# Performance work log

Hardware: AMD Instinct MI355X
Metric: run time of the kernel (lower is better)

## Reference

```python
import jax, jax.numpy as jnp
import numpy as np

B, Hh, Ww, C = 32, 56, 56, 256
WIN, SHIFT, HEADS = 7, 3, 8
N = WIN * WIN
nW = (Hh // WIN) * (Ww // WIN)


def _rel_pos_index(w):
    coords = np.stack(np.meshgrid(np.arange(w), np.arange(w), indexing='ij'))  # (2,w,w)
    flat = coords.reshape(2, -1)
    rel = (flat[:, :, None] - flat[:, None, :]).transpose(1, 2, 0)  # (N,N,2)
    rel[..., 0] += w - 1
    rel[..., 1] += w - 1
    rel[..., 0] *= 2 * w - 1
    return rel.sum(-1)  # (N,N) int


def _shift_attn_mask(H, W, w, s):
    img = np.zeros((H, W))
    cnt = 0
    for hs in (slice(0, -w), slice(-w, -s), slice(-s, None)):
        for ws in (slice(0, -w), slice(-w, -s), slice(-s, None)):
            img[hs, ws] = cnt
            cnt += 1
    mw = img.reshape(H // w, w, W // w, w).transpose(0, 2, 1, 3).reshape(-1, w * w)  # (nW,N)
    diff = mw[:, None, :] - mw[:, :, None]
    return np.where(diff != 0, -100.0, 0.0).astype(np.float32)  # (nW,N,N)


REL_IDX = jnp.asarray(_rel_pos_index(WIN))


def layer_norm(x, g, b):
    m = x.mean(-1, keepdims=True)
    v = ((x - m) ** 2).mean(-1, keepdims=True)
    return (x - m) / jnp.sqrt(v + 1e-5) * g + b


def setup_inputs() -> dict:
    key = jax.random.key(0)
    ks = jax.random.split(key, 10)
    s02 = 0.02
    x = jax.random.normal(ks[0], (B, Hh * Ww, C), jnp.float32)
    qkv_w = jax.random.normal(ks[1], (3 * C, C), jnp.float32) * s02
    qkv_b = jnp.zeros((3 * C,), jnp.float32)
    rpb_table = jax.random.normal(ks[2], ((2 * WIN - 1) ** 2, HEADS), jnp.float32) * s02
    proj_w = jax.random.normal(ks[3], (C, C), jnp.float32) * s02
    proj_b = jnp.zeros((C,), jnp.float32)
    fc1_w = jax.random.normal(ks[4], (4 * C, C), jnp.float32) * s02
    fc1_b = jnp.zeros((4 * C,), jnp.float32)
    fc2_w = jax.random.normal(ks[5], (C, 4 * C), jnp.float32) * s02
    fc2_b = jnp.zeros((C,), jnp.float32)
    attn_mask = jnp.asarray(_shift_attn_mask(Hh, Ww, WIN, SHIFT))
    # saliency masks: per-token binary fg/bg -> additive 0/-100 key masks
    fg_tok = jax.random.bernoulli(ks[6], 0.5, (B * nW, N))
    sal_fg = jnp.where(fg_tok[:, None, :], 0.0, -100.0) * jnp.ones((1, N, 1), jnp.float32)
    sal_bg = jnp.where(fg_tok[:, None, :], -100.0, 0.0) * jnp.ones((1, N, 1), jnp.float32)
    return dict(x=x, qkv_w=qkv_w, qkv_b=qkv_b, rpb_table=rpb_table, proj_w=proj_w,
                proj_b=proj_b, norm1_g=jnp.ones((C,)), norm1_b=jnp.zeros((C,)),
                norm2_g=jnp.ones((C,)), norm2_b=jnp.zeros((C,)),
                fc1_w=fc1_w, fc1_b=fc1_b, fc2_w=fc2_w, fc2_b=fc2_b,
                attn_mask=attn_mask, sal_fg_attn_mask=sal_fg.astype(jnp.float32),
                sal_bg_attn_mask=sal_bg.astype(jnp.float32))


def reference(x, qkv_w, qkv_b, rpb_table, proj_w, proj_b, norm1_g, norm1_b,
              norm2_g, norm2_b, fc1_w, fc1_b, fc2_w, fc2_b,
              attn_mask, sal_fg_attn_mask, sal_bg_attn_mask):
    Bb, L, Cc = x.shape
    d = Cc // HEADS
    scale = d ** -0.5
    shortcut = x
    xn = layer_norm(x, norm1_g, norm1_b).reshape(Bb, Hh, Ww, Cc)
    xs = jnp.roll(xn, (-SHIFT, -SHIFT), axis=(1, 2))
    # window partition -> (B*nW, N, C)
    nh = Hh // WIN
    xw = xs.reshape(Bb, nh, WIN, nh, WIN, Cc).transpose(0, 1, 3, 2, 4, 5).reshape(-1, N, Cc)
    B_ = xw.shape[0]
    qkv = (xw @ qkv_w.T + qkv_b).reshape(B_, N, 3, HEADS, d).transpose(2, 0, 3, 1, 4)
    q, k, v = qkv[0] * scale, qkv[1], qkv[2]  # (B_, h, N, d)
    attn = jnp.einsum('bhnd,bhmd->bhnm', q, k)
    rpb = rpb_table[REL_IDX.reshape(-1)].reshape(N, N, HEADS).transpose(2, 0, 1)
    attn = attn + rpb[None]
    attn_fg = attn + sal_fg_attn_mask[:, None]
    attn_bg = attn + sal_bg_attn_mask[:, None]

    def add_shift(a):
        a = a.reshape(B_ // nW, nW, HEADS, N, N) + attn_mask[None, :, None]
        return a.reshape(B_, HEADS, N, N)

    p = jax.nn.softmax(add_shift(attn), axis=-1)
    p_fg = jax.nn.softmax(add_shift(attn_fg), axis=-1)
    p_bg = jax.nn.softmax(add_shift(attn_bg), axis=-1)
    o = jnp.einsum('bhnm,bhmd->bhnd', p + p_fg - p_bg, v)
    o = o.transpose(0, 2, 1, 3).reshape(B_, N, Cc)
    o = o @ proj_w.T + proj_b
    # window reverse + reverse shift
    xr = o.reshape(Bb, nh, nh, WIN, WIN, Cc).transpose(0, 1, 3, 2, 4, 5).reshape(Bb, Hh, Ww, Cc)
    xr = jnp.roll(xr, (SHIFT, SHIFT), axis=(1, 2)).reshape(Bb, L, Cc)
    x = shortcut + xr
    h = layer_norm(x, norm2_g, norm2_b)
    h = jax.nn.gelu(h @ fc1_w.T + fc1_b, approximate=False) @ fc2_w.T + fc2_b
    return x + h
```

## Files before the change

kernel.cpp:

```cpp
#include <hip/hip_runtime.h>
#include <hip/hip_bf16.h>

#define HH 56
#define WWD 56
#define WIN 7
#define SHIFT 3
#define HEADS 8
#define NTOK 49
#define NW 64
#define CDIM 256
#define DH 32
#define MROWS 100352
#define SCALE_Q 0.17677669529663687f

typedef float floatx4 __attribute__((ext_vector_type(4)));
typedef __bf16 bf16x8 __attribute__((ext_vector_type(8)));

__device__ __forceinline__ float wave_sum(float v) {
#pragma unroll
    for (int m = 1; m < 64; m <<= 1) v += __shfl_xor(v, m);
    return v;
}

__device__ __forceinline__ void glds16(const void* g, void* l) {
    __builtin_amdgcn_global_load_lds(
        (const __attribute__((address_space(1))) void*)g,
        (__attribute__((address_space(3))) void*)l, 16, 0, 0);
}

__global__ __launch_bounds__(256) void convert_weights_kernel(
    const float* __restrict__ qkv_w, const float* __restrict__ proj_w,
    const float* __restrict__ fc1_w, const float* __restrict__ fc2_w,
    __hip_bfloat16* __restrict__ dst)
{
    int i = blockIdx.x * 256 + threadIdx.x;
    float v;
    if (i < 196608)       v = qkv_w[i];
    else if (i < 262144)  v = proj_w[i - 196608];
    else if (i < 524288)  v = fc1_w[i - 262144];
    else                  v = fc2_w[i - 524288];
    dst[i] = __float2bfloat16(v);
}

template <bool SHIFTED>
__global__ __launch_bounds__(256) void ln_kernel(
    const float* __restrict__ x, const float* __restrict__ g,
    const float* __restrict__ bb, __hip_bfloat16* __restrict__ out)
{
    const int tok  = blockIdx.x * 4 + (threadIdx.x >> 6);
    const int lane = threadIdx.x & 63;
    const int c    = lane * 4;

    float4 v = *reinterpret_cast<const float4*>(x + (size_t)tok * CDIM + c);
    float s = v.x + v.y + v.z + v.w;
    s = wave_sum(s);
    const float mean = s * (1.0f / 256.0f);
    float d0 = v.x - mean, d1 = v.y - mean, d2 = v.z - mean, d3 = v.w - mean;
    float sq = d0 * d0 + d1 * d1 + d2 * d2 + d3 * d3;
    sq = wave_sum(sq);
    const float rstd = rsqrtf(sq * (1.0f / 256.0f) + 1e-5f);

    float4 gv = *reinterpret_cast<const float4*>(g + c);
    float4 bv = *reinterpret_cast<const float4*>(bb + c);

    union { __hip_bfloat16 h[4]; uint2 u; } pk;
    pk.h[0] = __float2bfloat16(d0 * rstd * gv.x + bv.x);
    pk.h[1] = __float2bfloat16(d1 * rstd * gv.y + bv.y);
    pk.h[2] = __float2bfloat16(d2 * rstd * gv.z + bv.z);
    pk.h[3] = __float2bfloat16(d3 * rstd * gv.w + bv.w);

    size_t oidx;
    if (SHIFTED) {
        int b = tok / 3136;
        int l = tok - b * 3136;
        int h = l / WWD, w = l - (l / WWD) * WWD;
        int hp = h - SHIFT; if (hp < 0) hp += HH;
        int wp = w - SHIFT; if (wp < 0) wp += WWD;
        int bwin = b * NW + (hp / WIN) * 8 + (wp / WIN);
        int n = (hp % WIN) * WIN + (wp % WIN);
        oidx = ((size_t)bwin * NTOK + n) * CDIM + c;
    } else {
        oidx = (size_t)tok * CDIM + c;
    }
    *reinterpret_cast<uint2*>(out + oidx) = pk.u;
}

template <int MODE>
__global__ __launch_bounds__(256) void gemm_kernel(
    const __hip_bfloat16* __restrict__ A,
    const __hip_bfloat16* __restrict__ Wt,
    const float* __restrict__ bias,
    void* __restrict__ outv,
    const float* __restrict__ aux,
    int M, int Nn, int K)
{
    __shared__ __hip_bfloat16 As[3][128 * 32];
    __shared__ __hip_bfloat16 Bs[3][128 * 32];

    const int t = threadIdx.x;
    const int wave = t >> 6, lane = t & 63;

    const int nwg  = gridDim.x * gridDim.y;
    const int orig = blockIdx.y * gridDim.x + blockIdx.x;
    const int q = nwg >> 3, r = nwg & 7;
    const int xcd = orig & 7, loc = orig >> 3;
    const int lin = (xcd < r ? xcd * (q + 1) : r * (q + 1) + (xcd - r) * q) + loc;
    const int bx = lin % gridDim.x;
    const int by = lin / gridDim.x;

    const int m0 = by * 128, n0 = bx * 128;
    const int wr = (wave >> 1) * 64;
    const int wc = (wave & 1) * 64;

    floatx4 acc[4][4] = {};

    const int c0 = wave * 64 + lane;
    const int c1 = 256 + c0;
    const int r0 = c0 >> 2, p0 = c0 & 3, g0 = p0 ^ ((r0 >> 1) & 3);
    const int r1 = c1 >> 2, p1 = c1 & 3, g1 = p1 ^ ((r1 >> 1) & 3);
    const __hip_bfloat16* gA0 = A  + (size_t)(m0 + r0) * K + g0 * 8;
    const __hip_bfloat16* gA1 = A  + (size_t)(m0 + r1) * K + g1 * 8;
    const __hip_bfloat16* gB0 = Wt + (size_t)(n0 + r0) * K + g0 * 8;
    const __hip_bfloat16* gB1 = Wt + (size_t)(n0 + r1) * K + g1 * 8;
    const int base0 = (wave * 64) * 8;
    const int base1 = (256 + wave * 64) * 8;

    const int fm = lane & 15;
    const int g4 = lane >> 4;

    const int nt = K >> 5;

    glds16(gA0,      As[0] + base0);
    glds16(gA1,      As[0] + base1);
    glds16(gB0,      Bs[0] + base0);
    glds16(gB1,      Bs[0] + base1);
    glds16(gA0 + 32, As[1] + base0);
    glds16(gA1 + 32, As[1] + base1);
    glds16(gB0 + 32, Bs[1] + base0);
    glds16(gB1 + 32, Bs[1] + base1);
    asm volatile("s_waitcnt vmcnt(4)" ::: "memory");
    __builtin_amdgcn_s_barrier();
    __builtin_amdgcn_sched_barrier(0);

    int cur = 0;
    for (int tt = 0; tt < nt; ++tt) {
        if (tt + 2 < nt) {
            const int nx2 = (cur >= 1) ? cur - 1 : cur + 2;
            const int k2 = (tt + 2) << 5;
            glds16(gA0 + k2, As[nx2] + base0);
            glds16(gA1 + k2, As[nx2] + base1);
            glds16(gB0 + k2, Bs[nx2] + base0);
            glds16(gB1 + k2, Bs[nx2] + base1);
        }

        const __hip_bfloat16* Ac = As[cur];
        const __hip_bfloat16* Bc = Bs[cur];
        bf16x8 af[4], bfr[4];
#pragma unroll
        for (int mt = 0; mt < 4; ++mt) {
            const int ml = wr + mt * 16 + fm;
            af[mt] = *reinterpret_cast<const bf16x8*>(
                Ac + ml * 32 + ((g4 ^ ((ml >> 1) & 3)) * 8));
            const int nl = wc + mt * 16 + fm;
            bfr[mt] = *reinterpret_cast<const bf16x8*>(
                Bc + nl * 32 + ((g4 ^ ((nl >> 1) & 3)) * 8));
        }
#pragma unroll
        for (int mt = 0; mt < 4; ++mt)
#pragma unroll
            for (int nn = 0; nn < 4; ++nn)
                acc[mt][nn] = __builtin_amdgcn_mfma_f32_16x16x32_bf16(
                    af[mt], bfr[nn], acc[mt][nn], 0, 0, 0);

        if (tt + 1 < nt) {
            if (tt + 2 < nt)
                asm volatile("s_waitcnt vmcnt(4) lgkmcnt(0)" ::: "memory");
            else
                asm volatile("s_waitcnt vmcnt(0) lgkmcnt(0)" ::: "memory");
            __builtin_amdgcn_s_barrier();
            __builtin_amdgcn_sched_barrier(0);
        }
        cur = (cur >= 2) ? 0 : cur + 1;
    }

    float bv[4];
#pragma unroll
    for (int nn = 0; nn < 4; ++nn) bv[nn] = bias[n0 + wc + nn * 16 + fm];

#pragma unroll
    for (int mt = 0; mt < 4; ++mt) {
#pragma unroll
        for (int rr = 0; rr < 4; ++rr) {
            const int m_g = m0 + wr + mt * 16 + g4 * 4 + rr;
            size_t row_idx = 0;
            if (MODE == 1) {
                int bwin = m_g / NTOK;
                int ntok = m_g - bwin * NTOK;
                int b = bwin >> 6, wi = bwin & 63;
                int r2 = ntok / WIN, cc = ntok - r2 * WIN;
                int hp = (wi >> 3) * WIN + r2;
                int wp = (wi & 7) * WIN + cc;
                int h = hp + SHIFT; if (h >= HH) h -= HH;
                int w = wp + SHIFT; if (w >= WWD) w -= WWD;
                row_idx = ((size_t)b * 3136 + h * WWD + w) * CDIM;
            }
#pragma unroll
            for (int nn = 0; nn < 4; ++nn) {
                const int n_g = n0 + wc + nn * 16 + fm;
                float val = acc[mt][nn][rr] + bv[nn];
                if (MODE == 0) {
                    if (n_g < 256) val *= SCALE_Q;
                    reinterpret_cast<__hip_bfloat16*>(outv)[(size_t)m_g * Nn + n_g] =
                        __float2bfloat16(val);
                } else if (MODE == 2) {
                    float u  = val;
                    float y2 = 1.5957691216057308f * u
                             * (1.0f + 0.044715f * u * u);
                    float e  = __expf(y2);
                    float th = 1.0f - 2.0f / (e + 1.0f);
                    float gl = 0.5f * u * (1.0f + th);
                    reinterpret_cast<__hip_bfloat16*>(outv)[(size_t)m_g * Nn + n_g] =
                        __float2bfloat16(gl);
                } else if (MODE == 3) {
                    size_t idx = (size_t)m_g * CDIM + n_g;
                    reinterpret_cast<float*>(outv)[idx] = aux[idx] + val;
                } else {
                    size_t idx = row_idx + n_g;
                    reinterpret_cast<float*>(outv)[idx] = aux[idx] + val;
                }
            }
        }
    }
}

__global__ __launch_bounds__(256) void attn_kernel(
    const __hip_bfloat16* __restrict__ qkv,
    const float* __restrict__ rpb_table,
    const float* __restrict__ sal_fg,
    __hip_bfloat16* __restrict__ o)
{
    __shared__ unsigned short Pl[4][64 * 40];
    __shared__ unsigned short Vt[4][32 * 72];
    __shared__ float rpb_l[4][176];

    const int t = threadIdx.x;
    const int wave = t >> 6, lane = t & 63;
    const int lane15 = lane & 15, g4 = lane >> 4;
    const int b_ = blockIdx.x >> 1;
    const int h = ((blockIdx.x & 1) << 2) | wave;

    unsigned short* Pw = Pl[wave];
    unsigned short* Vw = Vt[wave];
    float* rpbw = rpb_l[wave];

    const unsigned short* qkv_u = reinterpret_cast<const unsigned short*>(qkv);
    const size_t base = (size_t)b_ * (NTOK * 768) + h * DH;

#pragma unroll
    for (int it = 0; it < 32; ++it) {
        int idx = it * 64 + lane;
        int key = idx >> 5, d = idx & 31;
        unsigned short v = (key < NTOK) ? qkv_u[base + key * 768 + 512 + d]
                                        : (unsigned short)0;
        Vw[d * 72 + key] = v;
    }
#pragma unroll
    for (int it = 0; it < 3; ++it) {
        int i = it * 64 + lane;
        if (i < 169) rpbw[i] = rpb_table[i * 8 + h];
    }
    float sfv = (lane < NTOK) ? sal_fg[(size_t)b_ * (NTOK * NTOK) + lane] : -100.f;
    const unsigned long long fgmask = __ballot(sfv == 0.0f);

    bf16x8 kf[4], qf[4];
#pragma unroll
    for (int mt = 0; mt < 4; ++mt)
        kf[mt] = *reinterpret_cast<const bf16x8*>(
            qkv_u + base + (size_t)(mt * 16 + lane15) * 768 + 256 + g4 * 8);
#pragma unroll
    for (int nt = 0; nt < 4; ++nt)
        qf[nt] = *reinterpret_cast<const bf16x8*>(
            qkv_u + base + (size_t)(nt * 16 + lane15) * 768 + g4 * 8);

    floatx4 S[4][4] = {};
#pragma unroll
    for (int mt = 0; mt < 4; ++mt)
#pragma unroll
        for (int nt = 0; nt < 4; ++nt)
            S[mt][nt] = __builtin_amdgcn_mfma_f32_16x16x32_bf16(
                kf[mt], qf[nt], S[mt][nt], 0, 0, 0);

    const int wr_ = (b_ & 63) >> 3, wc_ = (b_ & 63) & 7;
    int qlin[4], qreg[4];
#pragma unroll
    for (int nt = 0; nt < 4; ++nt) {
        int q = nt * 16 + lane15;
        int qr = (q * 147) >> 10, qc = q - qr * 7;
        qlin[nt] = q + 6 * qr + 84;
        qreg[nt] = ((wr_ == 7) ? ((qr < 4) ? 1 : 2) : 0) * 3
                 + ((wc_ == 7) ? ((qc < 4) ? 1 : 2) : 0);
    }

#pragma unroll
    for (int mt = 0; mt < 4; ++mt)
#pragma unroll
        for (int r = 0; r < 4; ++r) {
            int key = mt * 16 + g4 * 4 + r;
            int kr = (key * 147) >> 10, kc = key - kr * 7;
            int klin = key + 6 * kr;
            int kreg = ((wr_ == 7) ? ((kr < 4) ? 1 : 2) : 0) * 3
                     + ((wc_ == 7) ? ((kc < 4) ? 1 : 2) : 0);
            bool pad = key >= NTOK;
#pragma unroll
            for (int nt = 0; nt < 4; ++nt) {
                int idx = qlin[nt] - klin;
                idx = idx < 0 ? 0 : (idx > 168 ? 168 : idx);
                float s = S[mt][nt][r] + rpbw[idx]
                        + ((qreg[nt] == kreg) ? 0.f : -100.f);
                S[mt][nt][r] = pad ? -1e30f : s;
            }
        }

    float Cfg[4], Cbg[4];
#pragma unroll
    for (int nt = 0; nt < 4; ++nt) {
        float mfg = -3e38f, mbg = -3e38f;
#pragma unroll
        for (int mt = 0; mt < 4; ++mt)
#pragma unroll
            for (int r = 0; r < 4; ++r) {
                int key = mt * 16 + g4 * 4 + r;
                bool fg = (fgmask >> key) & 1ULL;
                float s = S[mt][nt][r];
                mfg = fg ? fmaxf(mfg, s) : mfg;
                mbg = fg ? mbg : fmaxf(mbg, s);
            }
        mfg = fmaxf(mfg, __shfl_xor(mfg, 16)); mfg = fmaxf(mfg, __shfl_xor(mfg, 32));
        mbg = fmaxf(mbg, __shfl_xor(mbg, 16)); mbg = fmaxf(mbg, __shfl_xor(mbg, 32));
        float t1 = 0.f, t2 = 0.f;
#pragma unroll
        for (int mt = 0; mt < 4; ++mt)
#pragma unroll
            for (int r = 0; r < 4; ++r) {
                int key = mt * 16 + g4 * 4 + r;
                bool fg = (fgmask >> key) & 1ULL;
                float e = __expf(S[mt][nt][r] - (fg ? mfg : mbg));
                S[mt][nt][r] = e;
                t1 += fg ? e : 0.f;
                t2 += fg ? 0.f : e;
            }
        t1 += __shfl_xor(t1, 16); t1 += __shfl_xor(t1, 32);
        t2 += __shfl_xor(t2, 16); t2 += __shfl_xor(t2, 32);
        const float m0 = fmaxf(mfg, mbg);
        const float m1 = fmaxf(mfg, mbg - 100.f);
        const float m2 = fmaxf(mfg - 100.f, mbg);
        const float a1 = __expf(mfg - m0),          a2 = __expf(mbg - m0);
        const float b1 = __expf(mfg - m1),          b2 = __expf(mbg - 100.f - m1);
        const float c1 = __expf(mfg - 100.f - m2),  c2 = __expf(mbg - m2);
        const float r0 = 1.f / (t1 * a1 + t2 * a2);
        const float r1 = 1.f / (t1 * b1 + t2 * b2);
        const float r2 = 1.f / (t1 * c1 + t2 * c2);
        Cfg[nt] = a1 * r0 + b1 * r1 - c1 * r2;
        Cbg[nt] = a2 * r0 + b2 * r1 - c2 * r2;
    }

    floatx4 Oc[4][2] = {};
#pragma unroll
    for (int kc = 0; kc < 2; ++kc) {
#pragma unroll
        for (int mh = 0; mh < 2; ++mh) {
            const int mt = kc * 2 + mh;
#pragma unroll
            for (int rp = 0; rp < 2; ++rp) {
                const int key0 = mt * 16 + g4 * 4 + 2 * rp;
                const bool fg0 = (fgmask >> key0) & 1ULL;
                const bool fg1 = (fgmask >> (key0 + 1)) & 1ULL;
                const int keyLocal = key0 - kc * 32;
#pragma unroll
                for (int nt = 0; nt < 4; ++nt) {
                    float pA = S[mt][nt][2 * rp]     * (fg0 ? Cfg[nt] : Cbg[nt]);
                    float pB = S[mt][nt][2 * rp + 1] * (fg1 ? Cfg[nt] : Cbg[nt]);
                    union { __hip_bfloat16 hh[2]; unsigned u; } pk;
                    pk.hh[0] = __float2bfloat16(pA);
                    pk.hh[1] = __float2bfloat16(pB);
                    const int q = nt * 16 + lane15;
                    *reinterpret_cast<unsigned*>(Pw + q * 40 + keyLocal) = pk.u;
                }
            }
        }
        bf16x8 pa[4], vb[2];
#pragma unroll
        for (int mtile = 0; mtile < 4; ++mtile)
            pa[mtile] = *reinterpret_cast<const bf16x8*>(
                Pw + (mtile * 16 + lane15) * 40 + g4 * 8);
#pragma unroll
        for (int n2 = 0; n2 < 2; ++n2)
            vb[n2] = *reinterpret_cast<const bf16x8*>(
                Vw + (n2 * 16 + lane15) * 72 + kc * 32 + g4 * 8);
#pragma unroll
        for (int mtile = 0; mtile < 4; ++mtile)
#pragma unroll
            for (int n2 = 0; n2 < 2; ++n2)
                Oc[mtile][n2] = __builtin_amdgcn_mfma_f32_16x16x32_bf16(
                    pa[mtile], vb[n2], Oc[mtile][n2], 0, 0, 0);
    }

#pragma unroll
    for (int mt = 0; mt < 4; ++mt)
#pragma unroll
        for (int r = 0; r < 4; ++r) {
            int query = mt * 16 + g4 * 4 + r;
            if (query < NTOK) {
                __hip_bfloat16* op = o + ((size_t)b_ * NTOK + query) * CDIM + h * DH;
#pragma unroll
                for (int n2 = 0; n2 < 2; ++n2)
                    op[n2 * 16 + lane15] = __float2bfloat16(Oc[mt][n2][r]);
            }
        }
}

extern "C" void kernel_launch(void* const* d_in, const int* in_sizes, int n_in,
                              void* d_out, int out_size, void* d_ws, size_t ws_size,
                              hipStream_t stream)
{
    const float* x        = (const float*)d_in[0];
    const float* qkv_w    = (const float*)d_in[1];
    const float* qkv_b    = (const float*)d_in[2];
    const float* rpb_tab  = (const float*)d_in[3];
    const float* proj_w   = (const float*)d_in[4];
    const float* proj_b   = (const float*)d_in[5];
    const float* n1g      = (const float*)d_in[6];
    const float* n1b      = (const float*)d_in[7];
    const float* n2g      = (const float*)d_in[8];
    const float* n2b      = (const float*)d_in[9];
    const float* fc1_w    = (const float*)d_in[10];
    const float* fc1_b    = (const float*)d_in[11];
    const float* fc2_w    = (const float*)d_in[12];
    const float* fc2_b    = (const float*)d_in[13];
    const float* sal_fg   = (const float*)d_in[15];

    char* ws = (char*)d_ws;
    __hip_bfloat16* regA = (__hip_bfloat16*)ws;
    __hip_bfloat16* regB = (__hip_bfloat16*)(ws + 205520896);
    float*          x2   = (float*)(ws + 205520896 + 51380224);
    __hip_bfloat16* wbf  = (__hip_bfloat16*)(ws + 205520896 + 51380224 + 102760448);
    __hip_bfloat16* wqkv  = wbf;
    __hip_bfloat16* wproj = wbf + 196608;
    __hip_bfloat16* wfc1  = wbf + 262144;
    __hip_bfloat16* wfc2  = wbf + 524288;

    convert_weights_kernel<<<3072, 256, 0, stream>>>(qkv_w, proj_w, fc1_w, fc2_w, wbf);

    ln_kernel<true><<<MROWS / 4, 256, 0, stream>>>(x, n1g, n1b, regB);

    gemm_kernel<0><<<dim3(768 / 128, MROWS / 128), 256, 0, stream>>>(
        regB, wqkv, qkv_b, regA, nullptr, MROWS, 768, 256);

    attn_kernel<<<2048 * 2, 256, 0, stream>>>(regA, rpb_tab, sal_fg, regB);

    gemm_kernel<1><<<dim3(256 / 128, MROWS / 128), 256, 0, stream>>>(
        regB, wproj, proj_b, x2, x, MROWS, 256, 256);

    ln_kernel<false><<<MROWS / 4, 256, 0, stream>>>(x2, n2g, n2b, regB);

    gemm_kernel<2><<<dim3(1024 / 128, MROWS / 128), 256, 0, stream>>>(
        regB, wfc1, fc1_b, regA, nullptr, MROWS, 1024, 256);

    gemm_kernel<3><<<dim3(256 / 128, MROWS / 128), 256, 0, stream>>>(
        regA, wfc2, fc2_b, d_out, x2, MROWS, 256, 1024);
}
```

Measured before the change: 701.4 us.

## Keep A tile resident in LDS across all N tiles; widen fc2 GEMM tile

The K=256 GEMMs now load a 128x256 A block into LDS once per workgroup and loop over every output column tile, streaming only weight tiles with double buffering. This removes the repeated reads of A that happen when separate workgroups handle each N tile. The fc2 GEMM uses a 128x256 output tile per workgroup so A is read only once, at the cost of more accumulator registers. The trade is 64KB+ of LDS per workgroup and a full barrier every k-step, which lowers occupancy and shortens the prefetch depth.

```diff
diff --git a/kernel.cpp b/kernel.cpp
--- a/kernel.cpp
+++ b/kernel.cpp
@@ -85,60 +85,186 @@
     *reinterpret_cast<uint2*>(out + oidx) = pk.u;
 }
 
-template <int MODE>
-__global__ __launch_bounds__(256) void gemm_kernel(
+template <int MODE, int NTILES>
+__global__ __launch_bounds__(256) void gemm_astat(
     const __hip_bfloat16* __restrict__ A,
     const __hip_bfloat16* __restrict__ Wt,
     const float* __restrict__ bias,
     void* __restrict__ outv,
     const float* __restrict__ aux,
-    int M, int Nn, int K)
+    int M, int Nn)
 {
-    __shared__ __hip_bfloat16 As[3][128 * 32];
-    __shared__ __hip_bfloat16 Bs[3][128 * 32];
-
-    const int t = threadIdx.x;
-    const int wave = t >> 6, lane = t & 63;
-
-    const int nwg  = gridDim.x * gridDim.y;
-    const int orig = blockIdx.y * gridDim.x + blockIdx.x;
-    const int q = nwg >> 3, r = nwg & 7;
-    const int xcd = orig & 7, loc = orig >> 3;
-    const int lin = (xcd < r ? xcd * (q + 1) : r * (q + 1) + (xcd - r) * q) + loc;
-    const int bx = lin % gridDim.x;
-    const int by = lin / gridDim.x;
-
-    const int m0 = by * 128, n0 = bx * 128;
+    __shared__ __hip_bfloat16 Asd[128 * 256];
+    __shared__ __hip_bfloat16 Wb[2][128 * 32];
+
+    const int tid = threadIdx.x;
+    const int wave = tid >> 6, lane = tid & 63;
+    const int m0 = blockIdx.x * 128;
+
+    const int fm = lane & 15;
+    const int g4 = lane >> 4;
     const int wr = (wave >> 1) * 64;
     const int wc = (wave & 1) * 64;
-
-    floatx4 acc[4][4] = {};
 
     const int c0 = wave * 64 + lane;
     const int c1 = 256 + c0;
     const int r0 = c0 >> 2, p0 = c0 & 3, g0 = p0 ^ ((r0 >> 1) & 3);
     const int r1 = c1 >> 2, p1 = c1 & 3, g1 = p1 ^ ((r1 >> 1) & 3);
-    const __hip_bfloat16* gA0 = A  + (size_t)(m0 + r0) * K + g0 * 8;
-    const __hip_bfloat16* gA1 = A  + (size_t)(m0 + r1) * K + g1 * 8;
-    const __hip_bfloat16* gB0 = Wt + (size_t)(n0 + r0) * K + g0 * 8;
-    const __hip_bfloat16* gB1 = Wt + (size_t)(n0 + r1) * K + g1 * 8;
-    const int base0 = (wave * 64) * 8;
-    const int base1 = (256 + wave * 64) * 8;
+    const int wbase0 = wave * 512;
+    const int wbase1 = 2048 + wave * 512;
+
+#pragma unroll
+    for (int i = 0; i < 16; ++i) {
+        const int idx = i * 256 + tid;
+        const int row = idx >> 5, b = idx & 31;
+        const int sc = b ^ (row & 7);
+        glds16(A + (size_t)(m0 + row) * 256 + sc * 8,
+               Asd + (i * 256 + wave * 64) * 8);
+    }
+    glds16(Wt + (size_t)r0 * 256 + g0 * 8, Wb[0] + wbase0);
+    glds16(Wt + (size_t)r1 * 256 + g1 * 8, Wb[0] + wbase1);
+
+    floatx4 acc[4][4] = {};
+    const int NT8 = NTILES * 8;
+
+    for (int t = 0; t < NT8; ++t) {
+        asm volatile("s_waitcnt vmcnt(0)" ::: "memory");
+        __builtin_amdgcn_s_barrier();
+        __builtin_amdgcn_sched_barrier(0);
+
+        const int p = t & 1;
+        if (t + 1 < NT8) {
+            const int t1 = t + 1;
+            const int n0t = (t1 >> 3) * 128;
+            const int kc = (t1 & 7) * 32;
+            glds16(Wt + (size_t)(n0t + r0) * 256 + kc + g0 * 8, Wb[1 - p] + wbase0);
+            glds16(Wt + (size_t)(n0t + r1) * 256 + kc + g1 * 8, Wb[1 - p] + wbase1);
+        }
+
+        const int ks = t & 7;
+        bf16x8 af[4], bfr[4];
+#pragma unroll
+        for (int mt = 0; mt < 4; ++mt) {
+            const int row = wr + mt * 16 + fm;
+            af[mt] = *reinterpret_cast<const bf16x8*>(
+                Asd + row * 256 + (((ks * 4 + g4) ^ (row & 7)) * 8));
+            const int nl = wc + mt * 16 + fm;
+            bfr[mt] = *reinterpret_cast<const bf16x8*>(
+                Wb[p] + nl * 32 + ((g4 ^ ((nl >> 1) & 3)) * 8));
+        }
+#pragma unroll
+        for (int mt = 0; mt < 4; ++mt)
+#pragma unroll
+            for (int nn = 0; nn < 4; ++nn)
+                acc[mt][nn] = __builtin_amdgcn_mfma_f32_16x16x32_bf16(
+                    af[mt], bfr[nn], acc[mt][nn], 0, 0, 0);
+
+        if (ks == 7) {
+            const int ti = t >> 3;
+            const int nbase = ti * 128;
+            float bv[4];
+#pragma unroll
+            for (int nn = 0; nn < 4; ++nn)
+                bv[nn] = bias[nbase + wc + nn * 16 + fm];
+#pragma unroll
+            for (int mt = 0; mt < 4; ++mt) {
+#pragma unroll
+                for (int rr = 0; rr < 4; ++rr) {
+                    const int m_g = m0 + wr + mt * 16 + g4 * 4 + rr;
+                    size_t row_idx = 0;
+                    if (MODE == 1) {
+                        int bwin = m_g / NTOK;
+                        int ntok = m_g - bwin * NTOK;
+                        int b = bwin >> 6, wi = bwin & 63;
+                        int r2 = ntok / WIN, cc = ntok - r2 * WIN;
+                        int hp = (wi >> 3) * WIN + r2;
+                        int wp = (wi & 7) * WIN + cc;
+                        int h = hp + SHIFT; if (h >= HH) h -= HH;
+                        int w = wp + SHIFT; if (w >= WWD) w -= WWD;
+                        row_idx = ((size_t)b * 3136 + h * WWD + w) * CDIM;
+                    }
+#pragma unroll
+                    for (int nn = 0; nn < 4; ++nn) {
+                        const int n_g = nbase + wc + nn * 16 + fm;
+                        float val = acc[mt][nn][rr] + bv[nn];
+                        if (MODE == 0) {
+                            if (n_g < 256) val *= SCALE_Q;
+                            reinterpret_cast<__hip_bfloat16*>(outv)[(size_t)m_g * Nn + n_g] =
+                                __float2bfloat16(val);
+                        } else if (MODE == 2) {
+                            float u  = val;
+                            float y2 = 1.5957691216057308f * u
+                                     * (1.0f + 0.044715f * u * u);
+                            float e  = __expf(y2);
+                            float th = 1.0f - 2.0f / (e + 1.0f);
+                            float gl = 0.5f * u * (1.0f + th);
+                            reinterpret_cast<__hip_bfloat16*>(outv)[(size_t)m_g * Nn + n_g] =
+                                __float2bfloat16(gl);
+                        } else {
+                            size_t idx = row_idx + n_g;
+                            reinterpret_cast<float*>(outv)[idx] = aux[idx] + val;
+                        }
+                        acc[mt][nn][rr] = 0.0f;
+                    }
+                }
+            }
+        }
+    }
+}
+
+__global__ __launch_bounds__(256, 2) void gemm_k1024(
+    const __hip_bfloat16* __restrict__ A,
+    const __hip_bfloat16* __restrict__ Wt,
+    const float* __restrict__ bias,
+    float* __restrict__ outv,
+    const float* __restrict__ aux)
+{
+    __shared__ __hip_bfloat16 As[3][128 * 32];
+    __shared__ __hip_bfloat16 Bs[3][256 * 32];
+
+    const int tid = threadIdx.x;
+    const int wave = tid >> 6, lane = tid & 63;
+    const int m0 = blockIdx.x * 128;
 
     const int fm = lane & 15;
     const int g4 = lane >> 4;
-
-    const int nt = K >> 5;
-
-    glds16(gA0,      As[0] + base0);
-    glds16(gA1,      As[0] + base1);
-    glds16(gB0,      Bs[0] + base0);
-    glds16(gB1,      Bs[0] + base1);
-    glds16(gA0 + 32, As[1] + base0);
-    glds16(gA1 + 32, As[1] + base1);
-    glds16(gB0 + 32, Bs[1] + base0);
-    glds16(gB1 + 32, Bs[1] + base1);
-    asm volatile("s_waitcnt vmcnt(4)" ::: "memory");
+    const int wr = (wave >> 1) * 64;
+    const int wc = (wave & 1) * 128;
+
+    floatx4 acc[4][8] = {};
+
+    const int c0 = wave * 64 + lane;
+    int rj[4], gj[4];
+#pragma unroll
+    for (int j = 0; j < 4; ++j) {
+        const int cj = j * 256 + c0;
+        rj[j] = cj >> 2;
+        const int pj = cj & 3;
+        gj[j] = pj ^ ((rj[j] >> 1) & 3);
+    }
+    const __hip_bfloat16* gA0 = A + (size_t)(m0 + rj[0]) * 1024 + gj[0] * 8;
+    const __hip_bfloat16* gA1 = A + (size_t)(m0 + rj[1]) * 1024 + gj[1] * 8;
+    const __hip_bfloat16* gB0 = Wt + (size_t)rj[0] * 1024 + gj[0] * 8;
+    const __hip_bfloat16* gB1 = Wt + (size_t)rj[1] * 1024 + gj[1] * 8;
+    const __hip_bfloat16* gB2 = Wt + (size_t)rj[2] * 1024 + gj[2] * 8;
+    const __hip_bfloat16* gB3 = Wt + (size_t)rj[3] * 1024 + gj[3] * 8;
+    const int ab0 = wave * 512, ab1 = 2048 + wave * 512;
+    const int bb0 = wave * 512, bb1 = 2048 + wave * 512;
+    const int bb2 = 4096 + wave * 512, bb3 = 6144 + wave * 512;
+
+    const int nt = 32;
+
+#pragma unroll
+    for (int pp = 0; pp < 2; ++pp) {
+        const int kp = pp << 5;
+        glds16(gA0 + kp, As[pp] + ab0);
+        glds16(gA1 + kp, As[pp] + ab1);
+        glds16(gB0 + kp, Bs[pp] + bb0);
+        glds16(gB1 + kp, Bs[pp] + bb1);
+        glds16(gB2 + kp, Bs[pp] + bb2);
+        glds16(gB3 + kp, Bs[pp] + bb3);
+    }
+    asm volatile("s_waitcnt vmcnt(6)" ::: "memory");
     __builtin_amdgcn_s_barrier();
     __builtin_amdgcn_sched_barrier(0);
 
@@ -147,34 +273,39 @@
         if (tt + 2 < nt) {
             const int nx2 = (cur >= 1) ? cur - 1 : cur + 2;
             const int k2 = (tt + 2) << 5;
-            glds16(gA0 + k2, As[nx2] + base0);
-            glds16(gA1 + k2, As[nx2] + base1);
-            glds16(gB0 + k2, Bs[nx2] + base0);
-            glds16(gB1 + k2, Bs[nx2] + base1);
+            glds16(gA0 + k2, As[nx2] + ab0);
+            glds16(gA1 + k2, As[nx2] + ab1);
+            glds16(gB0 + k2, Bs[nx2] + bb0);
+            glds16(gB1 + k2, Bs[nx2] + bb1);
+            glds16(gB2 + k2, Bs[nx2] + bb2);
+            glds16(gB3 + k2, Bs[nx2] + bb3);
         }
 
         const __hip_bfloat16* Ac = As[cur];
         const __hip_bfloat16* Bc = Bs[cur];
-        bf16x8 af[4], bfr[4];
+        bf16x8 af[4], bfr[8];
 #pragma unroll
         for (int mt = 0; mt < 4; ++mt) {
             const int ml = wr + mt * 16 + fm;
             af[mt] = *reinterpret_cast<const bf16x8*>(
                 Ac + ml * 32 + ((g4 ^ ((ml >> 1) & 3)) * 8));
-            const int nl = wc + mt * 16 + fm;
-            bfr[mt] = *reinterpret_cast<const bf16x8*>(
+        }
+#pragma unroll
+        for (int nn = 0; nn < 8; ++nn) {
+            const int nl = wc + nn * 16 + fm;
+            bfr[nn] = *reinterpret_cast<const bf16x8*>(
                 Bc + nl * 32 + ((g4 ^ ((nl >> 1) & 3)) * 8));
         }
 #pragma unroll
         for (int mt = 0; mt < 4; ++mt)
 #pragma unroll
-            for (int nn = 0; nn < 4; ++nn)
+            for (int nn = 0; nn < 8; ++nn)
                 acc[mt][nn] = __builtin_amdgcn_mfma_f32_16x16x32_bf16(
                     af[mt], bfr[nn], acc[mt][nn], 0, 0, 0);
 
         if (tt + 1 < nt) {
             if (tt + 2 < nt)
-                asm volatile("s_waitcnt vmcnt(4) lgkmcnt(0)" ::: "memory");
+                asm volatile("s_waitcnt vmcnt(6) lgkmcnt(0)" ::: "memory");
             else
                 asm volatile("s_waitcnt vmcnt(0) lgkmcnt(0)" ::: "memory");
             __builtin_amdgcn_s_barrier();
@@ -183,51 +314,20 @@
         cur = (cur >= 2) ? 0 : cur + 1;
     }
 
-    float bv[4];
-#pragma unroll
-    for (int nn = 0; nn < 4; ++nn) bv[nn] = bias[n0 + wc + nn * 16 + fm];
+    float bv[8];
+#pragma unroll
+    for (int nn = 0; nn < 8; ++nn) bv[nn] = bias[wc + nn * 16 + fm];
 
 #pragma unroll
     for (int mt = 0; mt < 4; ++mt) {
 #pragma unroll
         for (int rr = 0; rr < 4; ++rr) {
             const int m_g = m0 + wr + mt * 16 + g4 * 4 + rr;
-            size_t row_idx = 0;
-            if (MODE == 1) {
-                int bwin = m_g / NTOK;
-                int ntok = m_g - bwin * NTOK;
-                int b = bwin >> 6, wi = bwin & 63;
-                int r2 = ntok / WIN, cc = ntok - r2 * WIN;
-                int hp = (wi >> 3) * WIN + r2;
-                int wp = (wi & 7) * WIN + cc;
-                int h = hp + SHIFT; if (h >= HH) h -= HH;
-                int w = wp + SHIFT; if (w >= WWD) w -= WWD;
-                row_idx = ((size_t)b * 3136 + h * WWD + w) * CDIM;
-            }
-#pragma unroll
-            for (int nn = 0; nn < 4; ++nn) {
-                const int n_g = n0 + wc + nn * 16 + fm;
-                float val = acc[mt][nn][rr] + bv[nn];
-                if (MODE == 0) {
-                    if (n_g < 256) val *= SCALE_Q;
-                    reinterpret_cast<__hip_bfloat16*>(outv)[(size_t)m_g * Nn + n_g] =
-                        __float2bfloat16(val);
-                } else if (MODE == 2) {
-                    float u  = val;
-                    float y2 = 1.5957691216057308f * u
-                             * (1.0f + 0.044715f * u * u);
-                    float e  = __expf(y2);
-                    float th = 1.0f - 2.0f / (e + 1.0f);
-                    float gl = 0.5f * u * (1.0f + th);
-                    reinterpret_cast<__hip_bfloat16*>(outv)[(size_t)m_g * Nn + n_g] =
-                        __float2bfloat16(gl);
-                } else if (MODE == 3) {
-                    size_t idx = (size_t)m_g * CDIM + n_g;
-                    reinterpret_cast<float*>(outv)[idx] = aux[idx] + val;
-                } else {
-                    size_t idx = row_idx + n_g;
-                    reinterpret_cast<float*>(outv)[idx] = aux[idx] + val;
-                }
+#pragma unroll
+            for (int nn = 0; nn < 8; ++nn) {
+                const int n_g = wc + nn * 16 + fm;
+                const size_t idx = (size_t)m_g * CDIM + n_g;
+                outv[idx] = aux[idx] + acc[mt][nn][rr] + bv[nn];
             }
         }
     }
@@ -453,19 +553,18 @@
 
     ln_kernel<true><<<MROWS / 4, 256, 0, stream>>>(x, n1g, n1b, regB);
 
-    gemm_kernel<0><<<dim3(768 / 128, MROWS / 128), 256, 0, stream>>>(
-        regB, wqkv, qkv_b, regA, nullptr, MROWS, 768, 256);
+    gemm_astat<0, 6><<<MROWS / 128, 256, 0, stream>>>(
+        regB, wqkv, qkv_b, regA, nullptr, MROWS, 768);
 
     attn_kernel<<<2048 * 2, 256, 0, stream>>>(regA, rpb_tab, sal_fg, regB);
 
-    gemm_kernel<1><<<dim3(256 / 128, MROWS / 128), 256, 0, stream>>>(
-        regB, wproj, proj_b, x2, x, MROWS, 256, 256);
+    gemm_astat<1, 2><<<MROWS / 128, 256, 0, stream>>>(
+        regB, wproj, proj_b, x2, x, MROWS, 256);
 
     ln_kernel<false><<<MROWS / 4, 256, 0, stream>>>(x2, n2g, n2b, regB);
 
-    gemm_kernel<2><<<dim3(1024 / 128, MROWS / 128), 256, 0, stream>>>(
-        regB, wfc1, fc1_b, regA, nullptr, MROWS, 1024, 256);
-
-    gemm_kernel<3><<<dim3(256 / 128, MROWS / 128), 256, 0, stream>>>(
-        regA, wfc2, fc2_b, d_out, x2, MROWS, 256, 1024);
-}
+    gemm_astat<2, 8><<<MROWS / 128, 256, 0, stream>>>(
+        regB, wfc1, fc1_b, regA, nullptr, MROWS, 1024);
+
+    gemm_k1024<<<MROWS / 128, 256, 0, stream>>>(regA, wfc2, fc2_b, (float*)d_out, x2);
+}
```

New measurement: 791.2 us. 1.13x slower.
